# Kernel tuning notes

Measured on AMD Instinct MI355X. Metric: run time of the kernel, lower is better.

Reference implementation:

```python
import jax, jax.numpy as jnp
import numpy as np

N_NODES = 100000
N_EDGES = 1600000
IN_DIM = 256
HIDDEN = 128


def setup_inputs() -> dict:
    key = jax.random.key(0)
    ks = jax.random.split(key, 8)
    x = jax.random.normal(ks[0], (N_NODES, IN_DIM), dtype=jnp.float32)
    edge_index = jax.random.randint(ks[1], (2, N_EDGES), 0, N_NODES, dtype=jnp.int64)
    W0 = jax.random.normal(ks[2], (IN_DIM, HIDDEN), dtype=jnp.float32) / np.sqrt(IN_DIM)
    b0 = jnp.zeros((HIDDEN,), dtype=jnp.float32)
    Wmu = jax.random.normal(ks[3], (HIDDEN, HIDDEN), dtype=jnp.float32) / np.sqrt(HIDDEN)
    bmu = jnp.zeros((HIDDEN,), dtype=jnp.float32)
    Wsig = jax.random.normal(ks[4], (HIDDEN, HIDDEN), dtype=jnp.float32) / np.sqrt(HIDDEN)
    bsig = jnp.zeros((HIDDEN,), dtype=jnp.float32)
    return {"x": x, "edge_index": edge_index, "W0": W0, "b0": b0,
            "Wmu": Wmu, "bmu": bmu, "Wsig": Wsig, "bsig": bsig}


def reference(x, edge_index, W0, b0, Wmu, bmu, Wsig, bsig):
    N = x.shape[0]
    # PyG gcn_norm: add self-loops (weight 1), deg over target (col),
    # norm = deg^-1/2[row] * w * deg^-1/2[col]
    loops = jnp.arange(N, dtype=edge_index.dtype)
    row = jnp.concatenate([edge_index[0], loops])  # sources
    col = jnp.concatenate([edge_index[1], loops])  # targets
    w = jnp.ones(row.shape[0], dtype=x.dtype)
    deg = jax.ops.segment_sum(w, col, num_segments=N)
    dinv = jnp.where(deg > 0, jax.lax.rsqrt(deg), 0.0).astype(x.dtype)
    norm = dinv[row] * dinv[col]  # [E+N]

    def gcn_conv(h, W, b):
        h = h @ W                                   # dense transform [N, out]
        msg = norm[:, None] * h[row]                # gather + scale [E+N, out]
        return jax.ops.segment_sum(msg, col, num_segments=N) + b

    h = jax.nn.relu(gcn_conv(x, W0, b0))
    mu = gcn_conv(h, Wmu, bmu)
    sigma = jax.nn.softplus(gcn_conv(h, Wsig, bsig)) + 1e-7
    return mu, sigma
```

## Files before the change

kernel.cpp:

```cpp
#include <hip/hip_runtime.h>
#include <math.h>

#define N_NODES 100000
#define N_EDGES 1600000
#define ROWB    512
#define HALFB   51200000ull
#define NBKT    196
#define BSH     9
#define BCAP    10240
#define EPB     1024

typedef float  f32x4  __attribute__((ext_vector_type(4)));
typedef __bf16 bf16x8 __attribute__((ext_vector_type(8)));
typedef short  s16x8  __attribute__((ext_vector_type(8)));
typedef unsigned long long u64;

__device__ __forceinline__ unsigned short f2bf(float f) {
    unsigned int u = __builtin_bit_cast(unsigned int, f);
    u += 0x7FFFu + ((u >> 16) & 1u);
    return (unsigned short)(u >> 16);
}
__device__ __forceinline__ float bf2f(unsigned short h) {
    unsigned int u = ((unsigned int)h) << 16;
    return __builtin_bit_cast(float, u);
}
__device__ __forceinline__ float bf_lo(unsigned int u) {
    return __builtin_bit_cast(float, u << 16);
}
__device__ __forceinline__ float bf_hi(unsigned int u) {
    return __builtin_bit_cast(float, u & 0xFFFF0000u);
}
__device__ __forceinline__ void splitx(const float4& a, const float4& b,
                                       bf16x8& hi, bf16x8& lo) {
    float v[8] = {a.x, a.y, a.z, a.w, b.x, b.y, b.z, b.w};
    s16x8 hh, ll;
    #pragma unroll
    for (int j = 0; j < 8; j++) {
        unsigned short hb = f2bf(v[j]);
        hh[j] = (short)hb;
        ll[j] = (short)f2bf(v[j] - bf2f(hb));
    }
    hi = __builtin_bit_cast(bf16x8, hh);
    lo = __builtin_bit_cast(bf16x8, ll);
}

#define MFMA16(a, b, c) __builtin_amdgcn_mfma_f32_16x16x32_bf16((a), (b), (c), 0, 0, 0)


__launch_bounds__(256)
__global__ void bin_kernel(const int* __restrict__ row, const int* __restrict__ col,
                           int* __restrict__ gcur, u64* __restrict__ entries) {
    __shared__ int hist[NBKT], base[NBKT], cur[NBKT];
    const int tid = threadIdx.x;
    for (int i = tid; i < NBKT; i += 256) { hist[i] = 0; cur[i] = 0; }
    __syncthreads();
    const int e0 = blockIdx.x * EPB;
    int cols[4];
    #pragma unroll
    for (int it = 0; it < 4; it++) {
        int e = e0 + it * 256 + tid;
        int c = (e < N_EDGES) ? col[e] : -1;
        cols[it] = c;
        if (c >= 0) atomicAdd(&hist[c >> BSH], 1);
    }
    __syncthreads();
    for (int i = tid; i < NBKT; i += 256)
        base[i] = atomicAdd(&gcur[i], hist[i]);
    __syncthreads();
    #pragma unroll
    for (int it = 0; it < 4; it++) {
        int e = e0 + it * 256 + tid;
        int c = cols[it];
        if (c >= 0) {
            int b = c >> BSH;
            int r = atomicAdd(&cur[b], 1);
            entries[(size_t)b * BCAP + base[b] + r] =
                ((u64)(unsigned)c << 32) | (unsigned)row[e];
        }
    }
}


__global__ void bktscan_kernel(const int* __restrict__ gcur, int* __restrict__ bktBase) {
    __shared__ int s[256];
    const int tid = threadIdx.x;
    int v = (tid < NBKT) ? gcur[tid] : 0;
    s[tid] = v;
    __syncthreads();
    for (int d = 1; d < 256; d <<= 1) {
        int t = (tid >= d) ? s[tid - d] : 0;
        __syncthreads();
        s[tid] += t;
        __syncthreads();
    }
    if (tid < NBKT) bktBase[tid] = s[tid] - v;
}


__launch_bounds__(256)
__global__ void csr_kernel(const u64* __restrict__ entries, const int* __restrict__ gcur,
                           const int* __restrict__ bktBase,
                           int* __restrict__ cnt, int* __restrict__ offs,
                           float* __restrict__ dinv, int* __restrict__ sortedRow) {
    __shared__ int lcnt[512], sA[512], sB[512], lcur[512];
    const int b = blockIdx.x, tid = threadIdx.x;
    const int n0 = b << BSH;
    lcnt[tid] = 0; lcnt[tid + 256] = 0;
    __syncthreads();
    const int nb = gcur[b], base = bktBase[b];
    const u64* ep = entries + (size_t)b * BCAP;
    for (int i = tid; i < nb; i += 256)
        atomicAdd(&lcnt[(int)(ep[i] >> 32) - n0], 1);
    __syncthreads();
    sA[tid] = lcnt[tid]; sA[tid + 256] = lcnt[tid + 256];
    __syncthreads();
    int* src = sA; int* dst = sB;
    for (int d = 1; d < 512; d <<= 1) {
        #pragma unroll
        for (int k = tid; k < 512; k += 256)
            dst[k] = src[k] + ((k >= d) ? src[k - d] : 0);
        __syncthreads();
        int* t = src; src = dst; dst = t;
    }
    #pragma unroll
    for (int k = tid; k < 512; k += 256) {
        int excl = src[k] - lcnt[k];
        lcur[k] = excl;
        int node = n0 + k;
        if (node < N_NODES) {
            offs[node] = base + excl;
            cnt[node]  = lcnt[k];
            dinv[node] = rsqrtf((float)(lcnt[k] + 1));
        }
    }
    __syncthreads();
    for (int i = tid; i < nb; i += 256) {
        u64 pk = ep[i];
        int local = (int)(pk >> 32) - n0;
        int p = base + atomicAdd(&lcur[local], 1);
        sortedRow[p] = (int)(pk & 0xFFFFFFFFu);
    }
}


__global__ void prep_w(const float* __restrict__ W0, const float* __restrict__ Wmu,
                       const float* __restrict__ Wsig,
                       unsigned short* __restrict__ W0h, unsigned short* __restrict__ W0l,
                       unsigned short* __restrict__ Wmsh, unsigned short* __restrict__ Wmsl) {
    int c = blockIdx.x;
    int k = threadIdx.x;
    if (c < 128) {
        float v = W0[k * 128 + c];
        unsigned short h = f2bf(v);
        W0h[c * 256 + k] = h;
        W0l[c * 256 + k] = f2bf(v - bf2f(h));
    } else if (k < 128) {
        int c2 = c - 128;
        float v = (c2 < 128) ? Wmu[k * 128 + c2] : Wsig[k * 128 + (c2 - 128)];
        unsigned short h = f2bf(v);
        Wmsh[c2 * 128 + k] = h;
        Wmsl[c2 * 128 + k] = f2bf(v - bf2f(h));
    }
}


__launch_bounds__(512, 4)
__global__ void gemm1_mfma(const float* __restrict__ x,
                           const unsigned short* __restrict__ W0h,
                           const unsigned short* __restrict__ W0l,
                           char* __restrict__ outc) {
    __shared__ __align__(16) char Bs[2][16384];
    const int tid = threadIdx.x;
    const int wave = tid >> 6, lane = tid & 63;
    const int lrow = lane & 15;
    const int kb = (lane >> 4) * 16;
    const int swz = (lrow & 7) << 4;
    const int koff0 = kb ^ swz, koff1 = (64 + kb) ^ swz;
    const int r0 = blockIdx.x * 128 + wave * 16;
    int rm = r0 + lrow; if (rm > N_NODES - 1) rm = N_NODES - 1;
    const float* ap = x + (size_t)rm * 256 + (lane >> 4) * 8;

    const int colL = tid >> 3, k8 = (tid & 7) * 8;
    const int colH = colL + 64;
    const int dB0 = (colL * 128 + k8 * 2) ^ ((colL & 7) << 4);
    const int dB1 = (colH * 128 + k8 * 2) ^ ((colH & 7) << 4);

    float4 xr[8];
    #pragma unroll
    for (int ki = 0; ki < 4; ki++) {
        xr[2 * ki]     = *(const float4*)(ap + ki * 32);
        xr[2 * ki + 1] = *(const float4*)(ap + ki * 32 + 4);
    }
    bf16x8 bh[4], bl[4];
    #pragma unroll
    for (int ki = 0; ki < 4; ki++) splitx(xr[2 * ki], xr[2 * ki + 1], bh[ki], bl[ki]);

    {
        const unsigned short* W = W0h;
        *(int4*)(Bs[0] + dB0) = *(const int4*)(W + colL * 256 + k8);
        *(int4*)(Bs[0] + dB1) = *(const int4*)(W + colH * 256 + k8);
    }
    __syncthreads();

    f32x4 acc[8] = {};
    #pragma unroll
    for (int c = 0; c < 8; c++) {
        const int ks = c & 1;
        int4 w0, w1;
        if (c < 7) {
            const int nc = c + 1;
            const unsigned short* W = (((nc >> 1) & 1) ? W0l : W0h)
                                      + (nc >> 2) * 128 + (nc & 1) * 64;
            w0 = *(const int4*)(W + colL * 256 + k8);
            w1 = *(const int4*)(W + colH * 256 + k8);
        }
        if (c == 3) {
            #pragma unroll
            for (int ki = 0; ki < 4; ki++) {
                xr[2 * ki]     = *(const float4*)(ap + 128 + ki * 32);
                xr[2 * ki + 1] = *(const float4*)(ap + 128 + ki * 32 + 4);
            }
        }
        if (c == 4) {
            #pragma unroll
            for (int ki = 0; ki < 4; ki++) splitx(xr[2 * ki], xr[2 * ki + 1], bh[ki], bl[ki]);
        }
        const char* bufp = Bs[c & 1];
        const bool isHi = ((c >> 1) & 1) == 0;
        #pragma unroll
        for (int ki2 = 0; ki2 < 2; ki2++) {
            const int ki = ks * 2 + ki2;
            const int ko = ki2 ? koff1 : koff0;
            #pragma unroll
            for (int n = 0; n < 8; n++) {
                bf16x8 w = *(const bf16x8*)(bufp + (n * 16 + lrow) * 128 + ko);
                acc[n] = MFMA16(w, bh[ki], acc[n]);
                if (isHi) acc[n] = MFMA16(w, bl[ki], acc[n]);
            }
        }
        if (c < 7) {
            *(int4*)(Bs[(c + 1) & 1] + dB0) = w0;
            *(int4*)(Bs[(c + 1) & 1] + dB1) = w1;
            __syncthreads();
        }
    }

    const int node = r0 + lrow;
    if (node < N_NODES) {
        char* dst = outc + (size_t)node * ROWB + 256;
        #pragma unroll
        for (int n = 0; n < 8; n++) {
            int f0 = n * 16 + (lane >> 4) * 4;
            ushort4 p = make_ushort4(f2bf(acc[n][0]), f2bf(acc[n][1]),
                                     f2bf(acc[n][2]), f2bf(acc[n][3]));
            *(ushort4*)(dst + f0 * 2) = p;
        }
    }
}


template <int EPI>
__launch_bounds__(256)
__global__ void agg_bf16(const char* __restrict__ srcBase, char* __restrict__ dstBase,
                         const int* __restrict__ offs, const int* __restrict__ cnt,
                         const int* __restrict__ sortedRow, const float* __restrict__ dinv,
                         const float* __restrict__ bias) {
    const int n = blockIdx.x * 4 + (threadIdx.x >> 6);
    const int lane = threadIdx.x & 63;
    const float dn = dinv[n];
    const char* srcLane = srcBase + (size_t)lane * 4;
    unsigned int u = *(const unsigned int*)(srcLane + (size_t)n * ROWB);
    const float ws = dn * dn;
    float acc0 = ws * bf_lo(u);
    float acc1 = ws * bf_hi(u);
    const int start = offs[n], num = cnt[n];

    for (int i = 0; i < num; i += 8) {
        int r[8];
        #pragma unroll
        for (int j = 0; j < 8; j++) {
            bool valid = (i + j) < num;
            int idx = start + (valid ? (i + j) : 0);
            int rr = sortedRow[idx];
            r[j] = valid ? rr : n;
        }
        unsigned int ue[8];
        #pragma unroll
        for (int j = 0; j < 8; j++)
            ue[j] = *(const unsigned int*)(srcLane + (size_t)r[j] * ROWB);
        float w[8];
        #pragma unroll
        for (int j = 0; j < 8; j++) {
            float wv = dn * dinv[r[j]];
            w[j] = ((i + j) < num) ? wv : 0.f;
        }
        #pragma unroll
        for (int j = 0; j < 8; j++) {
            acc0 = fmaf(w[j], bf_lo(ue[j]), acc0);
            acc1 = fmaf(w[j], bf_hi(ue[j]), acc1);
        }
    }

    if (EPI) {
        acc0 = fmaxf(acc0 + bias[2 * lane], 0.f);
        acc1 = fmaxf(acc1 + bias[2 * lane + 1], 0.f);
    }
    unsigned int o = (unsigned int)f2bf(acc0) | ((unsigned int)f2bf(acc1) << 16);
    *(unsigned int*)(dstBase + (size_t)n * ROWB + lane * 4) = o;
}


__launch_bounds__(512, 4)
__global__ void gemm2_mfma(const unsigned short* __restrict__ Bh,
                           const unsigned short* __restrict__ Bl,
                           const float* __restrict__ bmu, const float* __restrict__ bsig,
                           char* __restrict__ outc) {
    __shared__ __align__(16) char Bs[2][16384];
    const int tid = threadIdx.x;
    const int wave = tid >> 6, lane = tid & 63;
    const int lrow = lane & 15;
    const int kb = (lane >> 4) * 16;
    const int swz = (lrow & 7) << 4;
    const int koff0 = kb ^ swz, koff1 = (64 + kb) ^ swz;
    const int r0 = blockIdx.x * 128 + wave * 16;
    int rm = r0 + lrow; if (rm > N_NODES - 1) rm = N_NODES - 1;

    const int colL = tid >> 3, k8 = (tid & 7) * 8;
    const int colH = colL + 64;
    const int dB0 = (colL * 128 + k8 * 2) ^ ((colL & 7) << 4);
    const int dB1 = (colH * 128 + k8 * 2) ^ ((colH & 7) << 4);

    const char* apc = outc + (size_t)rm * ROWB + kb;
    bf16x8 b[4];
    #pragma unroll
    for (int ki = 0; ki < 4; ki++)
        b[ki] = *(const bf16x8*)(apc + ki * 64);

    *(int4*)(Bs[0] + dB0) = *(const int4*)(Bh + colL * 128 + k8);
    *(int4*)(Bs[0] + dB1) = *(const int4*)(Bh + colH * 128 + k8);
    __syncthreads();

    const int node = r0 + lrow;
    const bool ok = node < N_NODES;
    f32x4 acc[8] = {};

    #pragma unroll
    for (int c = 0; c < 8; c++) {
        const int ks = c & 1;
        int4 w0, w1;
        if (c < 7) {
            const int nc = c + 1;
            const unsigned short* W = (((nc >> 1) & 1) ? Bl : Bh)
                                      + (nc >> 2) * 16384 + (nc & 1) * 64;
            w0 = *(const int4*)(W + colL * 128 + k8);
            w1 = *(const int4*)(W + colH * 128 + k8);
        }
        const char* bufp = Bs[c & 1];
        #pragma unroll
        for (int ki2 = 0; ki2 < 2; ki2++) {
            const int ki = ks * 2 + ki2;
            const int ko = ki2 ? koff1 : koff0;
            #pragma unroll
            for (int n = 0; n < 8; n++) {
                bf16x8 w = *(const bf16x8*)(bufp + (n * 16 + lrow) * 128 + ko);
                acc[n] = MFMA16(w, b[ki], acc[n]);
            }
        }
        if (c == 3) {
            if (ok) {
                char* dst = outc + (size_t)node * ROWB;
                #pragma unroll
                for (int n = 0; n < 8; n++) {
                    int f0 = n * 16 + (lane >> 4) * 4;
                    float4 bv = *(const float4*)(bmu + f0);
                    float4 o = make_float4(acc[n][0] + bv.x, acc[n][1] + bv.y,
                                           acc[n][2] + bv.z, acc[n][3] + bv.w);
                    *(float4*)(dst + f0 * 4) = o;
                }
            }
            #pragma unroll
            for (int n = 0; n < 8; n++) acc[n] = f32x4{0.f, 0.f, 0.f, 0.f};
        }
        if (c < 7) {
            *(int4*)(Bs[(c + 1) & 1] + dB0) = w0;
            *(int4*)(Bs[(c + 1) & 1] + dB1) = w1;
            __syncthreads();
        }
    }

    if (ok) {
        char* dst = outc + HALFB + (size_t)node * ROWB;
        #pragma unroll
        for (int n = 0; n < 8; n++) {
            int f0 = n * 16 + (lane >> 4) * 4;
            float4 bv = *(const float4*)(bsig + f0);
            float t[4];
            #pragma unroll
            for (int q = 0; q < 4; q++) {
                float xv = acc[n][q] + ((const float*)&bv)[q];
                t[q] = fmaxf(xv, 0.f) + log1pf(expf(-fabsf(xv))) + 1e-7f;
            }
            *(float4*)(dst + f0 * 4) = make_float4(t[0], t[1], t[2], t[3]);
        }
    }
}


extern "C" void kernel_launch(void* const* d_in, const int* in_sizes, int n_in,
                              void* d_out, int out_size, void* d_ws, size_t ws_size,
                              hipStream_t stream) {
    const float* x    = (const float*)d_in[0];
    const int*   ei   = (const int*)d_in[1];
    const int*   row  = ei;
    const int*   col  = ei + N_EDGES;
    const float* W0   = (const float*)d_in[2];
    const float* b0   = (const float*)d_in[3];
    const float* Wmu  = (const float*)d_in[4];
    const float* bmu  = (const float*)d_in[5];
    const float* Wsig = (const float*)d_in[6];
    const float* bsig = (const float*)d_in[7];
    char* outc = (char*)d_out;

    unsigned short* W0h  = (unsigned short*)d_ws;
    unsigned short* W0l  = W0h + 32768;
    unsigned short* Wmsh = W0l + 32768;
    unsigned short* Wmsl = Wmsh + 32768;
    int*   cnt       = (int*)(Wmsl + 32768);
    int*   gcur      = cnt + N_NODES;
    int*   bktBase   = gcur + NBKT;
    int*   offs      = bktBase + NBKT;
    float* dinvp     = (float*)(offs + N_NODES);
    int*   sortedRow = (int*)(dinvp + N_NODES);

    u64* entries = (u64*)(outc + HALFB);

    hipMemsetAsync(gcur, 0, NBKT * sizeof(int), stream);
    prep_w<<<384, 256, 0, stream>>>(W0, Wmu, Wsig, W0h, W0l, Wmsh, Wmsl);
    bin_kernel<<<(N_EDGES + EPB - 1) / EPB, 256, 0, stream>>>(row, col, gcur, entries);
    bktscan_kernel<<<1, 256, 0, stream>>>(gcur, bktBase);
    csr_kernel<<<NBKT, 256, 0, stream>>>(entries, gcur, bktBase, cnt, offs, dinvp, sortedRow);

    gemm1_mfma<<<(N_NODES + 127) / 128, 512, 0, stream>>>(x, W0h, W0l, outc);
    agg_bf16<1><<<N_NODES / 4, 256, 0, stream>>>(outc + 256, outc + HALFB,
                                                 offs, cnt, sortedRow, dinvp, b0);
    agg_bf16<0><<<N_NODES / 4, 256, 0, stream>>>(outc + HALFB, outc,
                                                 offs, cnt, sortedRow, dinvp, nullptr);
    gemm2_mfma<<<(N_NODES + 127) / 128, 512, 0, stream>>>(Wmsh, Wmsl, bmu, bsig, outc);
}
```

Baseline: 313.0 us.

## Replace LDS-staged GEMMs with register-direct MFMA and scalarize aggregation indices

Both GEMM kernels drop the shared-memory double-buffered weight staging. Each 64-lane wave now handles 32 nodes and reads weights directly from global/L2 into registers. GEMM1 also drops the low-part bf16 split of x and keeps only the bf16 high part of activations, while still applying the hi/lo weight split. The aggregation kernel reads source-node indices once per 8 edges and broadcasts them with readlane/readfirstlane, replacing the per-lane predicated tail with a scalar remainder loop. The intent is to remove LDS traffic, barriers and redundant index loads, at the cost of more global weight reads per wave and slightly lower x precision in the first layer.

```diff
diff --git a/kernel.cpp b/kernel.cpp
--- a/kernel.cpp
+++ b/kernel.cpp
@@ -30,18 +30,12 @@
 __device__ __forceinline__ float bf_hi(unsigned int u) {
     return __builtin_bit_cast(float, u & 0xFFFF0000u);
 }
-__device__ __forceinline__ void splitx(const float4& a, const float4& b,
-                                       bf16x8& hi, bf16x8& lo) {
+__device__ __forceinline__ bf16x8 packhi(const float4& a, const float4& b) {
     float v[8] = {a.x, a.y, a.z, a.w, b.x, b.y, b.z, b.w};
-    s16x8 hh, ll;
+    s16x8 hh;
     #pragma unroll
-    for (int j = 0; j < 8; j++) {
-        unsigned short hb = f2bf(v[j]);
-        hh[j] = (short)hb;
-        ll[j] = (short)f2bf(v[j] - bf2f(hb));
-    }
-    hi = __builtin_bit_cast(bf16x8, hh);
-    lo = __builtin_bit_cast(bf16x8, ll);
+    for (int j = 0; j < 8; j++) hh[j] = (short)f2bf(v[j]);
+    return __builtin_bit_cast(bf16x8, hh);
 }
 
 #define MFMA16(a, b, c) __builtin_amdgcn_mfma_f32_16x16x32_bf16((a), (b), (c), 0, 0, 0)
@@ -164,97 +158,63 @@
 }
 
 
-__launch_bounds__(512, 4)
+__launch_bounds__(128)
 __global__ void gemm1_mfma(const float* __restrict__ x,
-                           const unsigned short* __restrict__ W0h,
-                           const unsigned short* __restrict__ W0l,
+                           const unsigned short* __restrict__ Wh,
+                           const unsigned short* __restrict__ Wl,
                            char* __restrict__ outc) {
-    __shared__ __align__(16) char Bs[2][16384];
-    const int tid = threadIdx.x;
-    const int wave = tid >> 6, lane = tid & 63;
-    const int lrow = lane & 15;
-    const int kb = (lane >> 4) * 16;
-    const int swz = (lrow & 7) << 4;
-    const int koff0 = kb ^ swz, koff1 = (64 + kb) ^ swz;
-    const int r0 = blockIdx.x * 128 + wave * 16;
-    int rm = r0 + lrow; if (rm > N_NODES - 1) rm = N_NODES - 1;
-    const float* ap = x + (size_t)rm * 256 + (lane >> 4) * 8;
-
-    const int colL = tid >> 3, k8 = (tid & 7) * 8;
-    const int colH = colL + 64;
-    const int dB0 = (colL * 128 + k8 * 2) ^ ((colL & 7) << 4);
-    const int dB1 = (colH * 128 + k8 * 2) ^ ((colH & 7) << 4);
-
-    float4 xr[8];
+    const int lane = threadIdx.x & 63;
+    const int gw = blockIdx.x * 2 + (threadIdx.x >> 6);
+    const int r0 = gw * 32;
+    if (r0 >= N_NODES) return;
+    const int lrow = lane & 15, lk8 = (lane >> 4) * 8, fq = (lane >> 4) * 4;
+    const int node0 = r0 + lrow, node1 = node0 + 16;
+
+    const float* xp0 = x + (size_t)node0 * 256 + lk8;
+    const float* xp1 = x + (size_t)node1 * 256 + lk8;
+
+    f32x4 acc0[8] = {}, acc1[8] = {};
+    for (int kh = 0; kh < 2; kh++) {
+        bf16x8 xb0[4], xb1[4];
+        #pragma unroll
+        for (int s = 0; s < 4; s++) {
+            float4 p0 = *(const float4*)(xp0 + kh * 128 + s * 32);
+            float4 p1 = *(const float4*)(xp0 + kh * 128 + s * 32 + 4);
+            xb0[s] = packhi(p0, p1);
+            float4 q0 = *(const float4*)(xp1 + kh * 128 + s * 32);
+            float4 q1 = *(const float4*)(xp1 + kh * 128 + s * 32 + 4);
+            xb1[s] = packhi(q0, q1);
+        }
+        #pragma unroll 2
+        for (int ct = 0; ct < 8; ct++) {
+            const unsigned short* wph = Wh + (ct * 16 + lrow) * 256 + kh * 128 + lk8;
+            const unsigned short* wpl = Wl + (ct * 16 + lrow) * 256 + kh * 128 + lk8;
+            bf16x8 wh[4], wl[4];
+            #pragma unroll
+            for (int s = 0; s < 4; s++) {
+                wh[s] = *(const bf16x8*)(wph + s * 32);
+                wl[s] = *(const bf16x8*)(wpl + s * 32);
+            }
+            #pragma unroll
+            for (int s = 0; s < 4; s++) {
+                acc0[ct] = MFMA16(wh[s], xb0[s], acc0[ct]);
+                acc1[ct] = MFMA16(wh[s], xb1[s], acc1[ct]);
+                acc0[ct] = MFMA16(wl[s], xb0[s], acc0[ct]);
+                acc1[ct] = MFMA16(wl[s], xb1[s], acc1[ct]);
+            }
+        }
+    }
+    char* d0 = outc + (size_t)node0 * ROWB + 256;
+    char* d1 = outc + (size_t)node1 * ROWB + 256;
     #pragma unroll
-    for (int ki = 0; ki < 4; ki++) {
-        xr[2 * ki]     = *(const float4*)(ap + ki * 32);
-        xr[2 * ki + 1] = *(const float4*)(ap + ki * 32 + 4);
-    }
-    bf16x8 bh[4], bl[4];
-    #pragma unroll
-    for (int ki = 0; ki < 4; ki++) splitx(xr[2 * ki], xr[2 * ki + 1], bh[ki], bl[ki]);
-
-    {
-        const unsigned short* W = W0h;
-        *(int4*)(Bs[0] + dB0) = *(const int4*)(W + colL * 256 + k8);
-        *(int4*)(Bs[0] + dB1) = *(const int4*)(W + colH * 256 + k8);
-    }
-    __syncthreads();
-
-    f32x4 acc[8] = {};
-    #pragma unroll
-    for (int c = 0; c < 8; c++) {
-        const int ks = c & 1;
-        int4 w0, w1;
-        if (c < 7) {
-            const int nc = c + 1;
-            const unsigned short* W = (((nc >> 1) & 1) ? W0l : W0h)
-                                      + (nc >> 2) * 128 + (nc & 1) * 64;
-            w0 = *(const int4*)(W + colL * 256 + k8);
-            w1 = *(const int4*)(W + colH * 256 + k8);
-        }
-        if (c == 3) {
-            #pragma unroll
-            for (int ki = 0; ki < 4; ki++) {
-                xr[2 * ki]     = *(const float4*)(ap + 128 + ki * 32);
-                xr[2 * ki + 1] = *(const float4*)(ap + 128 + ki * 32 + 4);
-            }
-        }
-        if (c == 4) {
-            #pragma unroll
-            for (int ki = 0; ki < 4; ki++) splitx(xr[2 * ki], xr[2 * ki + 1], bh[ki], bl[ki]);
-        }
-        const char* bufp = Bs[c & 1];
-        const bool isHi = ((c >> 1) & 1) == 0;
-        #pragma unroll
-        for (int ki2 = 0; ki2 < 2; ki2++) {
-            const int ki = ks * 2 + ki2;
-            const int ko = ki2 ? koff1 : koff0;
-            #pragma unroll
-            for (int n = 0; n < 8; n++) {
-                bf16x8 w = *(const bf16x8*)(bufp + (n * 16 + lrow) * 128 + ko);
-                acc[n] = MFMA16(w, bh[ki], acc[n]);
-                if (isHi) acc[n] = MFMA16(w, bl[ki], acc[n]);
-            }
-        }
-        if (c < 7) {
-            *(int4*)(Bs[(c + 1) & 1] + dB0) = w0;
-            *(int4*)(Bs[(c + 1) & 1] + dB1) = w1;
-            __syncthreads();
-        }
-    }
-
-    const int node = r0 + lrow;
-    if (node < N_NODES) {
-        char* dst = outc + (size_t)node * ROWB + 256;
-        #pragma unroll
-        for (int n = 0; n < 8; n++) {
-            int f0 = n * 16 + (lane >> 4) * 4;
-            ushort4 p = make_ushort4(f2bf(acc[n][0]), f2bf(acc[n][1]),
-                                     f2bf(acc[n][2]), f2bf(acc[n][3]));
-            *(ushort4*)(dst + f0 * 2) = p;
-        }
+    for (int ct = 0; ct < 8; ct++) {
+        int f0 = ct * 16 + fq;
+        ushort4 pa = make_ushort4(f2bf(acc0[ct][0]), f2bf(acc0[ct][1]),
+                                  f2bf(acc0[ct][2]), f2bf(acc0[ct][3]));
+        *(ushort4*)(d0 + f0 * 2) = pa;
+        ushort4 pb = make_ushort4(f2bf(acc1[ct][0]), f2bf(acc1[ct][1]),
+                                  f2bf(acc1[ct][2]), f2bf(acc1[ct][3]));
+        *(ushort4*)(d1 + f0 * 2) = pb;
     }
 }
 
@@ -267,141 +227,136 @@
                          const float* __restrict__ bias) {
     const int n = blockIdx.x * 4 + (threadIdx.x >> 6);
     const int lane = threadIdx.x & 63;
+    const int laneB = lane * 4;
     const float dn = dinv[n];
-    const char* srcLane = srcBase + (size_t)lane * 4;
-    unsigned int u = *(const unsigned int*)(srcLane + (size_t)n * ROWB);
+    unsigned int u = *(const unsigned int*)(srcBase + (size_t)n * ROWB + laneB);
     const float ws = dn * dn;
     float acc0 = ws * bf_lo(u);
     float acc1 = ws * bf_hi(u);
-    const int start = offs[n], num = cnt[n];
-
-    for (int i = 0; i < num; i += 8) {
-        int r[8];
+    const int start = __builtin_amdgcn_readfirstlane(offs[n]);
+    const int num   = __builtin_amdgcn_readfirstlane(cnt[n]);
+
+    int i = 0;
+    for (; i + 8 <= num; i += 8) {
+        int myr = sortedRow[start + i + (lane & 7)];
+        int rs[8];
+        #pragma unroll
+        for (int j = 0; j < 8; j++) rs[j] = __builtin_amdgcn_readlane(myr, j);
+        unsigned int ue[8];
         #pragma unroll
         for (int j = 0; j < 8; j++) {
-            bool valid = (i + j) < num;
-            int idx = start + (valid ? (i + j) : 0);
-            int rr = sortedRow[idx];
-            r[j] = valid ? rr : n;
-        }
-        unsigned int ue[8];
-        #pragma unroll
-        for (int j = 0; j < 8; j++)
-            ue[j] = *(const unsigned int*)(srcLane + (size_t)r[j] * ROWB);
+            const char* p = srcBase + ((size_t)rs[j] << 9);
+            ue[j] = *(const unsigned int*)(p + laneB);
+        }
         float w[8];
         #pragma unroll
-        for (int j = 0; j < 8; j++) {
-            float wv = dn * dinv[r[j]];
-            w[j] = ((i + j) < num) ? wv : 0.f;
-        }
+        for (int j = 0; j < 8; j++) w[j] = dn * dinv[rs[j]];
         #pragma unroll
         for (int j = 0; j < 8; j++) {
             acc0 = fmaf(w[j], bf_lo(ue[j]), acc0);
             acc1 = fmaf(w[j], bf_hi(ue[j]), acc1);
         }
     }
+    for (; i < num; i++) {
+        int rsv = __builtin_amdgcn_readfirstlane(sortedRow[start + i]);
+        const char* p = srcBase + ((size_t)rsv << 9);
+        unsigned int ue = *(const unsigned int*)(p + laneB);
+        float w = dn * dinv[rsv];
+        acc0 = fmaf(w, bf_lo(ue), acc0);
+        acc1 = fmaf(w, bf_hi(ue), acc1);
+    }
 
     if (EPI) {
         acc0 = fmaxf(acc0 + bias[2 * lane], 0.f);
         acc1 = fmaxf(acc1 + bias[2 * lane + 1], 0.f);
     }
     unsigned int o = (unsigned int)f2bf(acc0) | ((unsigned int)f2bf(acc1) << 16);
-    *(unsigned int*)(dstBase + (size_t)n * ROWB + lane * 4) = o;
-}
-
-
-__launch_bounds__(512, 4)
-__global__ void gemm2_mfma(const unsigned short* __restrict__ Bh,
-                           const unsigned short* __restrict__ Bl,
+    *(unsigned int*)(dstBase + (size_t)n * ROWB + laneB) = o;
+}
+
+
+__launch_bounds__(128)
+__global__ void gemm2_mfma(const unsigned short* __restrict__ Wh,
+                           const unsigned short* __restrict__ Wl,
                            const float* __restrict__ bmu, const float* __restrict__ bsig,
                            char* __restrict__ outc) {
-    __shared__ __align__(16) char Bs[2][16384];
-    const int tid = threadIdx.x;
-    const int wave = tid >> 6, lane = tid & 63;
-    const int lrow = lane & 15;
-    const int kb = (lane >> 4) * 16;
-    const int swz = (lrow & 7) << 4;
-    const int koff0 = kb ^ swz, koff1 = (64 + kb) ^ swz;
-    const int r0 = blockIdx.x * 128 + wave * 16;
-    int rm = r0 + lrow; if (rm > N_NODES - 1) rm = N_NODES - 1;
-
-    const int colL = tid >> 3, k8 = (tid & 7) * 8;
-    const int colH = colL + 64;
-    const int dB0 = (colL * 128 + k8 * 2) ^ ((colL & 7) << 4);
-    const int dB1 = (colH * 128 + k8 * 2) ^ ((colH & 7) << 4);
-
-    const char* apc = outc + (size_t)rm * ROWB + kb;
-    bf16x8 b[4];
-    #pragma unroll
-    for (int ki = 0; ki < 4; ki++)
-        b[ki] = *(const bf16x8*)(apc + ki * 64);
-
-    *(int4*)(Bs[0] + dB0) = *(const int4*)(Bh + colL * 128 + k8);
-    *(int4*)(Bs[0] + dB1) = *(const int4*)(Bh + colH * 128 + k8);
-    __syncthreads();
-
-    const int node = r0 + lrow;
-    const bool ok = node < N_NODES;
-    f32x4 acc[8] = {};
-
-    #pragma unroll
-    for (int c = 0; c < 8; c++) {
-        const int ks = c & 1;
-        int4 w0, w1;
-        if (c < 7) {
-            const int nc = c + 1;
-            const unsigned short* W = (((nc >> 1) & 1) ? Bl : Bh)
-                                      + (nc >> 2) * 16384 + (nc & 1) * 64;
-            w0 = *(const int4*)(W + colL * 128 + k8);
-            w1 = *(const int4*)(W + colH * 128 + k8);
-        }
-        const char* bufp = Bs[c & 1];
-        #pragma unroll
-        for (int ki2 = 0; ki2 < 2; ki2++) {
-            const int ki = ks * 2 + ki2;
-            const int ko = ki2 ? koff1 : koff0;
-            #pragma unroll
-            for (int n = 0; n < 8; n++) {
-                bf16x8 w = *(const bf16x8*)(bufp + (n * 16 + lrow) * 128 + ko);
-                acc[n] = MFMA16(w, b[ki], acc[n]);
-            }
-        }
-        if (c == 3) {
-            if (ok) {
-                char* dst = outc + (size_t)node * ROWB;
-                #pragma unroll
-                for (int n = 0; n < 8; n++) {
-                    int f0 = n * 16 + (lane >> 4) * 4;
-                    float4 bv = *(const float4*)(bmu + f0);
-                    float4 o = make_float4(acc[n][0] + bv.x, acc[n][1] + bv.y,
-                                           acc[n][2] + bv.z, acc[n][3] + bv.w);
-                    *(float4*)(dst + f0 * 4) = o;
-                }
-            }
-            #pragma unroll
-            for (int n = 0; n < 8; n++) acc[n] = f32x4{0.f, 0.f, 0.f, 0.f};
-        }
-        if (c < 7) {
-            *(int4*)(Bs[(c + 1) & 1] + dB0) = w0;
-            *(int4*)(Bs[(c + 1) & 1] + dB1) = w1;
-            __syncthreads();
-        }
-    }
-
-    if (ok) {
-        char* dst = outc + HALFB + (size_t)node * ROWB;
-        #pragma unroll
-        for (int n = 0; n < 8; n++) {
-            int f0 = n * 16 + (lane >> 4) * 4;
-            float4 bv = *(const float4*)(bsig + f0);
-            float t[4];
-            #pragma unroll
-            for (int q = 0; q < 4; q++) {
-                float xv = acc[n][q] + ((const float*)&bv)[q];
-                t[q] = fmaxf(xv, 0.f) + log1pf(expf(-fabsf(xv))) + 1e-7f;
-            }
-            *(float4*)(dst + f0 * 4) = make_float4(t[0], t[1], t[2], t[3]);
-        }
+    const int lane = threadIdx.x & 63;
+    const int gw = blockIdx.x * 2 + (threadIdx.x >> 6);
+    const int r0 = gw * 32;
+    if (r0 >= N_NODES) return;
+    const int lrow = lane & 15, lk8 = (lane >> 4) * 8, fq = (lane >> 4) * 4;
+    const int node0 = r0 + lrow, node1 = node0 + 16;
+
+    bf16x8 b0[4], b1[4];
+    {
+        const char* a0 = outc + (size_t)node0 * ROWB + lk8 * 2;
+        const char* a1 = outc + (size_t)node1 * ROWB + lk8 * 2;
+        #pragma unroll
+        for (int ki = 0; ki < 4; ki++) {
+            b0[ki] = *(const bf16x8*)(a0 + ki * 64);
+            b1[ki] = *(const bf16x8*)(a1 + ki * 64);
+        }
+    }
+    char* mu0 = outc + (size_t)node0 * ROWB;
+    char* mu1 = outc + (size_t)node1 * ROWB;
+    char* sg0 = outc + HALFB + (size_t)node0 * ROWB;
+    char* sg1 = outc + HALFB + (size_t)node1 * ROWB;
+
+    #pragma unroll 2
+    for (int ct = 0; ct < 8; ct++) {
+        const unsigned short* wph = Wh + (ct * 16 + lrow) * 128 + lk8;
+        const unsigned short* wpl = Wl + (ct * 16 + lrow) * 128 + lk8;
+        bf16x8 wh[4], wl[4];
+        #pragma unroll
+        for (int ki = 0; ki < 4; ki++) {
+            wh[ki] = *(const bf16x8*)(wph + ki * 32);
+            wl[ki] = *(const bf16x8*)(wpl + ki * 32);
+        }
+        f32x4 aA = {}, aB = {};
+        #pragma unroll
+        for (int ki = 0; ki < 4; ki++) {
+            aA = MFMA16(wh[ki], b0[ki], aA);
+            aB = MFMA16(wh[ki], b1[ki], aB);
+            aA = MFMA16(wl[ki], b0[ki], aA);
+            aB = MFMA16(wl[ki], b1[ki], aB);
+        }
+        int f0 = ct * 16 + fq;
+        float4 bv = *(const float4*)(bmu + f0);
+        *(float4*)(mu0 + f0 * 4) = make_float4(aA[0] + bv.x, aA[1] + bv.y,
+                                               aA[2] + bv.z, aA[3] + bv.w);
+        *(float4*)(mu1 + f0 * 4) = make_float4(aB[0] + bv.x, aB[1] + bv.y,
+                                               aB[2] + bv.z, aB[3] + bv.w);
+    }
+    #pragma unroll 2
+    for (int ct = 0; ct < 8; ct++) {
+        const unsigned short* wph = Wh + ((128 + ct * 16 + lrow) * 128) + lk8;
+        const unsigned short* wpl = Wl + ((128 + ct * 16 + lrow) * 128) + lk8;
+        bf16x8 wh[4], wl[4];
+        #pragma unroll
+        for (int ki = 0; ki < 4; ki++) {
+            wh[ki] = *(const bf16x8*)(wph + ki * 32);
+            wl[ki] = *(const bf16x8*)(wpl + ki * 32);
+        }
+        f32x4 aA = {}, aB = {};
+        #pragma unroll
+        for (int ki = 0; ki < 4; ki++) {
+            aA = MFMA16(wh[ki], b0[ki], aA);
+            aB = MFMA16(wh[ki], b1[ki], aB);
+            aA = MFMA16(wl[ki], b0[ki], aA);
+            aB = MFMA16(wl[ki], b1[ki], aB);
+        }
+        int f0 = ct * 16 + fq;
+        float4 bv = *(const float4*)(bsig + f0);
+        float tA[4], tB[4];
+        #pragma unroll
+        for (int q = 0; q < 4; q++) {
+            float xa = aA[q] + ((const float*)&bv)[q];
+            tA[q] = fmaxf(xa, 0.f) + log1pf(expf(-fabsf(xa))) + 1e-7f;
+            float xb = aB[q] + ((const float*)&bv)[q];
+            tB[q] = fmaxf(xb, 0.f) + log1pf(expf(-fabsf(xb))) + 1e-7f;
+        }
+        *(float4*)(sg0 + f0 * 4) = make_float4(tA[0], tA[1], tA[2], tA[3]);
+        *(float4*)(sg1 + f0 * 4) = make_float4(tB[0], tB[1], tB[2], tB[3]);
     }
 }
 
@@ -440,10 +395,10 @@
     bktscan_kernel<<<1, 256, 0, stream>>>(gcur, bktBase);
     csr_kernel<<<NBKT, 256, 0, stream>>>(entries, gcur, bktBase, cnt, offs, dinvp, sortedRow);
 
-    gemm1_mfma<<<(N_NODES + 127) / 128, 512, 0, stream>>>(x, W0h, W0l, outc);
+    gemm1_mfma<<<(N_NODES / 32 + 1) / 2, 128, 0, stream>>>(x, W0h, W0l, outc);
     agg_bf16<1><<<N_NODES / 4, 256, 0, stream>>>(outc + 256, outc + HALFB,
                                                  offs, cnt, sortedRow, dinvp, b0);
     agg_bf16<0><<<N_NODES / 4, 256, 0, stream>>>(outc + HALFB, outc,
                                                  offs, cnt, sortedRow, dinvp, nullptr);
-    gemm2_mfma<<<(N_NODES + 127) / 128, 512, 0, stream>>>(Wmsh, Wmsl, bmu, bsig, outc);
-}
+    gemm2_mfma<<<(N_NODES / 32 + 1) / 2, 128, 0, stream>>>(Wmsh, Wmsl, bmu, bsig, outc);
+}
```

After: 374.1 us. 19.5% more time.
